# Optimization experiments

Hardware: AMD Instinct MI355X
Metric: run time of the kernel (lower is better)

Reference implementation:

```python
import jax, jax.numpy as jnp
import numpy as np

CTX = (16, 16)          # rel_pos_ctx_size
N_HEADS = 12
HEAD_DIM = 64           # emb_dim // n_heads


def _make_rel_pos_ids(ctx):
    # Faithful replication of the torch buffer construction.
    rge = [2 * s - 1 for s in ctx]
    coords = np.stack(np.meshgrid(*[np.arange(s) for s in ctx], indexing='ij'))  # [2, *ctx]
    coords = coords.reshape(len(ctx), -1)                                        # [2, n]
    rel = coords[:, :, None] - coords[:, None, :]                                # [2, n, n]
    rel = rel.reshape(len(ctx), -1)                                              # [2, n*n]
    rel = rel + (np.array(ctx)[:, None] - 1)
    ids = np.ravel_multi_index(tuple(rel), tuple(rge))                           # [n*n]
    return jnp.asarray(ids, dtype=jnp.int32)


def setup_inputs() -> dict:
    key = jax.random.key(0)
    ks = jax.random.split(key, 6)
    b, n, e = 128, 256, 768
    std_in = 1.0 / np.sqrt(e)
    return {
        'x': jax.random.normal(ks[0], (b, n, e), jnp.float32),
        'W_qkv': jax.random.normal(ks[1], (e, 3 * e), jnp.float32) * std_in,
        'b_qkv': jax.random.normal(ks[2], (3 * e,), jnp.float32) * 0.02,
        'W_out': jax.random.normal(ks[3], (e, e), jnp.float32) * std_in,
        'b_out': jax.random.normal(ks[4], (e,), jnp.float32) * 0.02,
        'rel_bias_table': jax.random.normal(ks[5], ((2 * CTX[0] - 1) * (2 * CTX[1] - 1), N_HEADS), jnp.float32) * 0.02,
        'rel_pos_ids': _make_rel_pos_ids(CTX),
    }


def reference(x, W_qkv, b_qkv, W_out, b_out, rel_bias_table, rel_pos_ids):
    b, n, e = x.shape
    h, d = N_HEADS, HEAD_DIM
    scale = d ** -0.5
    # fused qkv projection: 'b n (k h d) -> k b h n d'
    qkv = (x @ W_qkv + b_qkv).reshape(b, n, 3, h, d)
    q, k, v = (jnp.transpose(qkv, (2, 0, 3, 1, 4))[i] for i in range(3))  # each [b h n d]
    # gathered relative-position bias: [n*n, h] -> [h, n, n]
    bias = rel_bias_table[rel_pos_ids].reshape(n, n, h).transpose(2, 0, 1)
    scores = jnp.einsum('bhnd,bhmd->bhnm', q, k) * scale + bias
    attn = jax.nn.softmax(scores, axis=-1)
    out = jnp.einsum('bhnm,bhmd->bhnd', attn, v)
    out = out.transpose(0, 2, 1, 3).reshape(b, n, e)  # 'b h n d -> b n (h d)'
    return out @ W_out + b_out
```

## Files before the change

### kernel.cpp

```cpp
#include <hip/hip_runtime.h>
#include <cstdint>
#include <cstddef>

typedef __bf16 bf16x8 __attribute__((ext_vector_type(8)));
typedef __bf16 bf16x4 __attribute__((ext_vector_type(4)));
typedef float f32x4 __attribute__((ext_vector_type(4)));
static_assert(sizeof(bf16x8) == 16, "bf16x8 must be 16B");
static_assert(sizeof(bf16x4) == 8, "bf16x4 must be 8B");
static_assert(sizeof(f32x4) == 16, "f32x4 must be 16B");

#define MFMA16(a, b, c) __builtin_amdgcn_mfma_f32_16x16x32_bf16((a), (b), (c), 0, 0, 0)
#define SBAR() __builtin_amdgcn_s_barrier()
#define LGKM0() asm volatile("s_waitcnt lgkmcnt(0)" ::: "memory")
#define VMCNT(n_) asm volatile("s_waitcnt vmcnt(" #n_ ")" ::: "memory")

__device__ __forceinline__ void gload_lds16(const void* g, void* l) {
  __builtin_amdgcn_global_load_lds(
      (const __attribute__((address_space(1))) void*)g,
      (__attribute__((address_space(3))) void*)l, 16, 0, 0);
}

__global__ __launch_bounds__(256) void prep_kernel(
    const float* __restrict__ x, __bf16* __restrict__ xbf,
    const float* __restrict__ Wqkv, __bf16* __restrict__ wqkvt,
    const float* __restrict__ Wout, __bf16* __restrict__ woutt,
    const float* __restrict__ table, const int* __restrict__ ids,
    float* __restrict__ biasT) {
  __shared__ float tile[32][33];
  const int bid = blockIdx.x;
  const int tid = threadIdx.x;

  if (bid < 24576) {
    size_t i = ((size_t)bid * 256 + tid) * 4;
    const float4 v = *(const float4*)(x + i);
    bf16x4 pk;
    pk[0] = (__bf16)v.x;
    pk[1] = (__bf16)v.y;
    pk[2] = (__bf16)v.z;
    pk[3] = (__bf16)v.w;
    *(bf16x4*)(xbf + i) = pk;
  } else if (bid < 26880) {
    const bool big = bid < 26304;
    const int b2 = big ? (bid - 24576) : (bid - 26304);
    const int nt = big ? 72 : 24;
    const int N = big ? 2304 : 768;
    const float* in = big ? Wqkv : Wout;
    __bf16* out = big ? wqkvt : woutt;
    const int n0 = (b2 % nt) * 32, k0 = (b2 / nt) * 32;
    const int tx = tid & 31, ty = tid >> 5;
#pragma unroll
    for (int i = 0; i < 4; ++i)
      tile[ty * 4 + i][tx] = in[(size_t)(k0 + ty * 4 + i) * N + n0 + tx];
    __syncthreads();
#pragma unroll
    for (int i = 0; i < 4; ++i)
      out[(size_t)(n0 + ty * 4 + i) * 768 + k0 + tx] = (__bf16)tile[tx][ty * 4 + i];
  } else {
    const int idx = (bid - 26880) * 256 + tid;
    const int h = idx >> 16, ji = idx & 65535;
    const int j = ji >> 8, i = ji & 255;
    biasT[idx] = table[ids[i * 256 + j] * 12 + h];
  }
}

template <int NT>
__global__ __launch_bounds__(512, 2) void gemm8_qkv_kernel(const __bf16* __restrict__ A,
                                                           const __bf16* __restrict__ Bt,
                                                           const float* __restrict__ bias,
                                                           __bf16* __restrict__ qb,
                                                           __bf16* __restrict__ kb,
                                                           __bf16* __restrict__ vt,
                                                           const int M, const int K) {
  __shared__ __align__(16) __bf16 smem[65536];
  const int tid = threadIdx.x;
  const int lane = tid & 63, w = tid >> 6;
  const int m16 = lane & 15, q4 = lane >> 4;
  const int wm = w & 1, wn = w >> 1;

  const int nwg = NT * (M >> 8);
  const int chunk = nwg >> 3;
  const int id = blockIdx.x;
  const int wg = (id & 7) * chunk + (id >> 3);
  const int mi = wg / NT, ni = wg - mi * NT;
  const int m0 = mi << 8, n0 = ni << 8;

  const int srow = w * 8 + (lane >> 3);
  const int sg = ((lane & 7) ^ (srow & 7)) * 8;
  const __bf16* ag = A + (size_t)(m0 + srow) * K + sg;
  const __bf16* bg = Bt + (size_t)(n0 + srow) * K + sg;
  const int dstw = w * 512;

  const int g0 = (q4 ^ (m16 & 7)) * 8;
  const int g1 = ((4 + q4) ^ (m16 & 7)) * 8;
  const int abase = (wm * 128 + m16) * 64;
  const int bbase = 16384 + (wn * 64 + m16) * 64;

  const int nt = K >> 6;

#define STAGE(T_, mat_, h_)                                                         \
  do {                                                                              \
    const __bf16* s_ = ((mat_) ? bg : ag) + (size_t)(T_)*64 + (size_t)(h_)*128 * K; \
    __bf16* d_ = &smem[((T_)&1) * 32768 + (mat_)*16384 + (h_)*8192 + dstw];         \
    gload_lds16(s_, d_);                                                            \
    gload_lds16(s_ + (size_t)64 * K, d_ + 4096);                                    \
  } while (0)

  STAGE(0, 0, 0);
  STAGE(0, 0, 1);
  STAGE(0, 1, 0);
  STAGE(0, 1, 1);
  STAGE(1, 0, 0);
  VMCNT(2);
  SBAR();

  f32x4 acc[8][4] = {};
  for (int T = 0; T < nt; ++T) {
    const int base = (T & 1) * 32768;
    bf16x8 a[4][2], b0[2][2], b1[2][2];

#pragma unroll
    for (int fm = 0; fm < 4; ++fm) {
      a[fm][0] = *(const bf16x8*)&smem[base + abase + fm * 1024 + g0];
      a[fm][1] = *(const bf16x8*)&smem[base + abase + fm * 1024 + g1];
    }
#pragma unroll
    for (int fn = 0; fn < 2; ++fn) {
      b0[fn][0] = *(const bf16x8*)&smem[base + bbase + fn * 1024 + g0];
      b0[fn][1] = *(const bf16x8*)&smem[base + bbase + fn * 1024 + g1];
    }
    if (T + 1 < nt) {
      STAGE(T + 1, 0, 1);
      STAGE(T + 1, 1, 0);
      STAGE(T + 1, 1, 1);
    }
    SBAR();
    LGKM0();
    __builtin_amdgcn_s_setprio(1);
#pragma unroll
    for (int kh = 0; kh < 2; ++kh)
#pragma unroll
      for (int fm = 0; fm < 4; ++fm)
#pragma unroll
        for (int fn = 0; fn < 2; ++fn)
          acc[fm][fn] = MFMA16(b0[fn][kh], a[fm][kh], acc[fm][fn]);
    __builtin_amdgcn_s_setprio(0);
    SBAR();

#pragma unroll
    for (int fn = 0; fn < 2; ++fn) {
      b1[fn][0] = *(const bf16x8*)&smem[base + bbase + 2048 + fn * 1024 + g0];
      b1[fn][1] = *(const bf16x8*)&smem[base + bbase + 2048 + fn * 1024 + g1];
    }
    SBAR();
    LGKM0();
    __builtin_amdgcn_s_setprio(1);
#pragma unroll
    for (int kh = 0; kh < 2; ++kh)
#pragma unroll
      for (int fm = 0; fm < 4; ++fm)
#pragma unroll
        for (int fn = 0; fn < 2; ++fn)
          acc[fm][2 + fn] = MFMA16(b1[fn][kh], a[fm][kh], acc[fm][2 + fn]);
    __builtin_amdgcn_s_setprio(0);
    SBAR();

#pragma unroll
    for (int fm = 0; fm < 4; ++fm) {
      a[fm][0] = *(const bf16x8*)&smem[base + abase + 4096 + fm * 1024 + g0];
      a[fm][1] = *(const bf16x8*)&smem[base + abase + 4096 + fm * 1024 + g1];
    }
    SBAR();
    LGKM0();
    __builtin_amdgcn_s_setprio(1);
#pragma unroll
    for (int kh = 0; kh < 2; ++kh)
#pragma unroll
      for (int fm = 0; fm < 4; ++fm)
#pragma unroll
        for (int fn = 0; fn < 2; ++fn)
          acc[4 + fm][2 + fn] = MFMA16(b1[fn][kh], a[fm][kh], acc[4 + fm][2 + fn]);
    __builtin_amdgcn_s_setprio(0);
    SBAR();

    if (T + 2 < nt) {
      STAGE(T + 2, 0, 0);
      VMCNT(2);
    } else if (T + 1 < nt) {
      VMCNT(0);
    }
    SBAR();
    __builtin_amdgcn_s_setprio(1);
#pragma unroll
    for (int kh = 0; kh < 2; ++kh)
#pragma unroll
      for (int fm = 0; fm < 4; ++fm)
#pragma unroll
        for (int fn = 0; fn < 2; ++fn)
          acc[4 + fm][fn] = MFMA16(b0[fn][kh], a[fm][kh], acc[4 + fm][fn]);
    __builtin_amdgcn_s_setprio(0);
    SBAR();
  }
#undef STAGE

  __syncthreads();
  const int bi = m0 >> 8;
  char* eb = (char*)smem;

  if (n0 < 1536) {
    const int which = (n0 >= 768);
    const float qscale = which ? 1.0f : 0.125f;
#pragma unroll
    for (int fn = 0; fn < 4; ++fn) {
      const int nloc = wn * 64 + fn * 16 + q4 * 4;
      const f32x4 bn = *(const f32x4*)&bias[n0 + nloc];
      const int cb = nloc * 2;
      const int slot = cb >> 4;
      const int half8 = cb & 15;
#pragma unroll
      for (int fm = 0; fm < 8; ++fm) {
        const int tok = wm * 128 + fm * 16 + m16;
        bf16x4 pk;
#pragma unroll
        for (int r = 0; r < 4; ++r) pk[r] = (__bf16)((acc[fm][fn][r] + bn[r]) * qscale);
        *(bf16x4*)(eb + tok * 512 + ((slot ^ (tok & 7)) << 4) + half8) = pk;
      }
    }
    __syncthreads();
    const int nrel0 = n0 - which * 768;
    __bf16* dst = (which ? kb : qb) + (size_t)bi * 12 * 16384;
#pragma unroll
    for (int pass = 0; pass < 16; ++pass) {
      const int tokr = pass * 16 + (tid >> 5);
      const int slot = tid & 31;
      const bf16x8 vv = *(const bf16x8*)(eb + tokr * 512 + ((slot ^ (tokr & 7)) << 4));
      const int nr = nrel0 + slot * 8;
      *(bf16x8*)(dst + (size_t)(nr >> 6) * 16384 + (size_t)tokr * 64 + (nr & 63)) = vv;
    }
  } else {
#pragma unroll
    for (int fn = 0; fn < 4; ++fn)
#pragma unroll
      for (int r = 0; r < 4; ++r) {
        const int nloc = wn * 64 + fn * 16 + q4 * 4 + r;
        const float bn = bias[n0 + nloc];
#pragma unroll
        for (int fm = 0; fm < 8; ++fm) {
          const int tok = wm * 128 + fm * 16 + m16;
          const int tcb = tok * 2;
          *(__bf16*)(eb + nloc * 512 + (((tcb >> 4) ^ (nloc & 7)) << 4) + (tcb & 15)) =
              (__bf16)(acc[fm][fn][r] + bn);
        }
      }
    __syncthreads();
    const int nrel0v = n0 - 1536;
#pragma unroll
    for (int pass = 0; pass < 16; ++pass) {
      const int nr = pass * 16 + (tid >> 5);
      const int slot = tid & 31;
      const bf16x8 vv = *(const bf16x8*)(eb + nr * 512 + ((slot ^ (nr & 7)) << 4));
      const int ng = nrel0v + nr;
      *(bf16x8*)(vt + (((size_t)bi * 12 + (ng >> 6)) * 64 + (ng & 63)) * 256 + slot * 8) = vv;
    }
  }
}

template <int NT>
__global__ __launch_bounds__(512, 2) void gemm8_out_kernel(const __bf16* __restrict__ A,
                                                           const __bf16* __restrict__ Bt,
                                                           const float* __restrict__ bias,
                                                           float* __restrict__ out,
                                                           const int M, const int N,
                                                           const int K) {
  __shared__ __align__(16) __bf16 smem[65536];
  const int tid = threadIdx.x;
  const int lane = tid & 63, w = tid >> 6;
  const int m16 = lane & 15, q4 = lane >> 4;
  const int wm = w & 1, wn = w >> 1;

  const int nwg = NT * (M >> 8);
  const int chunk = nwg >> 3;
  const int id = blockIdx.x;
  const int wg = (id & 7) * chunk + (id >> 3);
  const int mi = wg / NT, ni = wg - mi * NT;
  const int m0 = mi << 8, n0 = ni << 8;

  const int srow = w * 8 + (lane >> 3);
  const int sg = ((lane & 7) ^ (srow & 7)) * 8;
  const __bf16* ag = A + (size_t)(m0 + srow) * K + sg;
  const __bf16* bg = Bt + (size_t)(n0 + srow) * K + sg;
  const int dstw = w * 512;

  const int g0 = (q4 ^ (m16 & 7)) * 8;
  const int g1 = ((4 + q4) ^ (m16 & 7)) * 8;
  const int abase = (wm * 128 + m16) * 64;
  const int bbase = 16384 + (wn * 64 + m16) * 64;

  const int nt = K >> 6;

#define STAGE(T_, mat_, h_)                                                         \
  do {                                                                              \
    const __bf16* s_ = ((mat_) ? bg : ag) + (size_t)(T_)*64 + (size_t)(h_)*128 * K; \
    __bf16* d_ = &smem[((T_)&1) * 32768 + (mat_)*16384 + (h_)*8192 + dstw];         \
    gload_lds16(s_, d_);                                                            \
    gload_lds16(s_ + (size_t)64 * K, d_ + 4096);                                    \
  } while (0)

  STAGE(0, 0, 0);
  STAGE(0, 0, 1);
  STAGE(0, 1, 0);
  STAGE(0, 1, 1);
  STAGE(1, 0, 0);
  VMCNT(2);
  SBAR();

  f32x4 acc[8][4] = {};
  for (int T = 0; T < nt; ++T) {
    const int base = (T & 1) * 32768;
    bf16x8 a[4][2], b0[2][2], b1[2][2];

#pragma unroll
    for (int fm = 0; fm < 4; ++fm) {
      a[fm][0] = *(const bf16x8*)&smem[base + abase + fm * 1024 + g0];
      a[fm][1] = *(const bf16x8*)&smem[base + abase + fm * 1024 + g1];
    }
#pragma unroll
    for (int fn = 0; fn < 2; ++fn) {
      b0[fn][0] = *(const bf16x8*)&smem[base + bbase + fn * 1024 + g0];
      b0[fn][1] = *(const bf16x8*)&smem[base + bbase + fn * 1024 + g1];
    }
    if (T + 1 < nt) {
      STAGE(T + 1, 0, 1);
      STAGE(T + 1, 1, 0);
      STAGE(T + 1, 1, 1);
    }
    SBAR();
    LGKM0();
    __builtin_amdgcn_s_setprio(1);
#pragma unroll
    for (int kh = 0; kh < 2; ++kh)
#pragma unroll
      for (int fm = 0; fm < 4; ++fm)
#pragma unroll
        for (int fn = 0; fn < 2; ++fn)
          acc[fm][fn] = MFMA16(b0[fn][kh], a[fm][kh], acc[fm][fn]);
    __builtin_amdgcn_s_setprio(0);
    SBAR();

#pragma unroll
    for (int fn = 0; fn < 2; ++fn) {
      b1[fn][0] = *(const bf16x8*)&smem[base + bbase + 2048 + fn * 1024 + g0];
      b1[fn][1] = *(const bf16x8*)&smem[base + bbase + 2048 + fn * 1024 + g1];
    }
    SBAR();
    LGKM0();
    __builtin_amdgcn_s_setprio(1);
#pragma unroll
    for (int kh = 0; kh < 2; ++kh)
#pragma unroll
      for (int fm = 0; fm < 4; ++fm)
#pragma unroll
        for (int fn = 0; fn < 2; ++fn)
          acc[fm][2 + fn] = MFMA16(b1[fn][kh], a[fm][kh], acc[fm][2 + fn]);
    __builtin_amdgcn_s_setprio(0);
    SBAR();

#pragma unroll
    for (int fm = 0; fm < 4; ++fm) {
      a[fm][0] = *(const bf16x8*)&smem[base + abase + 4096 + fm * 1024 + g0];
      a[fm][1] = *(const bf16x8*)&smem[base + abase + 4096 + fm * 1024 + g1];
    }
    SBAR();
    LGKM0();
    __builtin_amdgcn_s_setprio(1);
#pragma unroll
    for (int kh = 0; kh < 2; ++kh)
#pragma unroll
      for (int fm = 0; fm < 4; ++fm)
#pragma unroll
        for (int fn = 0; fn < 2; ++fn)
          acc[4 + fm][2 + fn] = MFMA16(b1[fn][kh], a[fm][kh], acc[4 + fm][2 + fn]);
    __builtin_amdgcn_s_setprio(0);
    SBAR();

    if (T + 2 < nt) {
      STAGE(T + 2, 0, 0);
      VMCNT(2);
    } else if (T + 1 < nt) {
      VMCNT(0);
    }
    SBAR();
    __builtin_amdgcn_s_setprio(1);
#pragma unroll
    for (int kh = 0; kh < 2; ++kh)
#pragma unroll
      for (int fm = 0; fm < 4; ++fm)
#pragma unroll
        for (int fn = 0; fn < 2; ++fn)
          acc[4 + fm][fn] = MFMA16(b0[fn][kh], a[fm][kh], acc[4 + fm][fn]);
    __builtin_amdgcn_s_setprio(0);
    SBAR();
  }
#undef STAGE

  __syncthreads();
  char* ef = (char*)smem;
#pragma unroll
  for (int half = 0; half < 2; ++half) {
    if ((wn >> 1) == half) {
#pragma unroll
      for (int fn = 0; fn < 4; ++fn) {
        const int nl = (wn & 1) * 64 + fn * 16 + q4 * 4;
        const f32x4 bn = *(const f32x4*)&bias[n0 + half * 128 + nl];
        const int slot = nl >> 2;
#pragma unroll
        for (int fm = 0; fm < 8; ++fm) {
          const int tok = wm * 128 + fm * 16 + m16;
          f32x4 v;
#pragma unroll
          for (int r = 0; r < 4; ++r) v[r] = acc[fm][fn][r] + bn[r];
          *(f32x4*)(ef + tok * 512 + ((slot ^ (tok & 7)) << 4)) = v;
        }
      }
    }
    __syncthreads();
#pragma unroll
    for (int pass = 0; pass < 16; ++pass) {
      const int tokr = pass * 16 + (tid >> 5);
      const int slot = tid & 31;
      const f32x4 vv = *(const f32x4*)(ef + tokr * 512 + ((slot ^ (tokr & 7)) << 4));
      *(f32x4*)(out + (size_t)(m0 + tokr) * N + n0 + half * 128 + slot * 4) = vv;
    }
    __syncthreads();
  }
}

__global__ __launch_bounds__(512, 4) void attn_kernel(const __bf16* __restrict__ qb,
                                                      const __bf16* __restrict__ kb,
                                                      const __bf16* __restrict__ vtb,
                                                      const float* __restrict__ biasT,
                                                      __bf16* __restrict__ o_ws) {
  __shared__ __bf16 klds[256 * 64];
  __shared__ __bf16 vlds[64 * 256];
  const int tid = threadIdx.x;
  const int lane = tid & 63, w = tid >> 6;
  const int m16 = lane & 15, q4 = lane >> 4;
  const int b = blockIdx.x, h = blockIdx.y;
  const size_t bh = (size_t)b * 12 + h;
  const __bf16* Q = qb + bh * (256 * 64);
  const __bf16* Kp = kb + bh * (256 * 64);
  const __bf16* Vt = vtb + bh * (64 * 256);
  const float* BhT = biasT + (size_t)h * 65536;
  const int qbase = blockIdx.z * 128;
  const int qrow0 = qbase + w * 16;

#pragma unroll
  for (int i = 0; i < 4; ++i) {
    const int row = w * 32 + i * 8 + (lane >> 3);
    const int col = ((lane & 7) ^ (row & 7)) * 8;
    gload_lds16(Kp + (size_t)row * 64 + col, &klds[(w * 32 + i * 8) * 64]);
  }
#pragma unroll
  for (int i = 0; i < 4; ++i) {
    const int row = w * 8 + i * 2 + (lane >> 5);
    const int g = lane & 31;
    const int gp = (g & 24) | ((g & 7) ^ (row & 7));
    gload_lds16(Vt + (size_t)row * 256 + gp * 8, &vlds[(w * 8 + i * 2) * 256]);
  }

  bf16x8 qf[2];
#pragma unroll
  for (int t = 0; t < 2; ++t)
    qf[t] = *(const bf16x8*)(Q + (size_t)(qrow0 + m16) * 64 + t * 32 + q4 * 8);

  __syncthreads();

  f32x4 s[16];
#pragma unroll
  for (int c = 0; c < 16; ++c) {
    const int krow = c * 16 + m16;
    const bf16x8 kf0 = *(const bf16x8*)&klds[krow * 64 + ((q4 ^ (m16 & 7)) * 8)];
    const bf16x8 kf1 = *(const bf16x8*)&klds[krow * 64 + (((4 + q4) ^ (m16 & 7)) * 8)];
    f32x4 z = {0.f, 0.f, 0.f, 0.f};
    z = MFMA16(qf[0], kf0, z);
    s[c] = MFMA16(qf[1], kf1, z);
  }

#pragma unroll
  for (int c = 0; c < 16; ++c) {
    const f32x4 bv = *(const f32x4*)&BhT[(size_t)(c * 16 + m16) * 256 + qrow0 + q4 * 4];
    s[c] += bv;
  }

  float linv[4];
#pragma unroll
  for (int r = 0; r < 4; ++r) {
    float mx = s[0][r];
#pragma unroll
    for (int c = 1; c < 16; ++c) mx = fmaxf(mx, s[c][r]);
    mx = fmaxf(mx, __shfl_xor(mx, 1));
    mx = fmaxf(mx, __shfl_xor(mx, 2));
    mx = fmaxf(mx, __shfl_xor(mx, 4));
    mx = fmaxf(mx, __shfl_xor(mx, 8));
    float sum = 0.f;
#pragma unroll
    for (int c = 0; c < 16; ++c) {
      const float p = __builtin_amdgcn_exp2f((s[c][r] - mx) * 1.4426950408889634f);
      s[c][r] = p;
      sum += p;
    }
    sum += __shfl_xor(sum, 1);
    sum += __shfl_xor(sum, 2);
    sum += __shfl_xor(sum, 4);
    sum += __shfl_xor(sum, 8);
    linv[r] = 1.f / sum;
  }

  __syncthreads();

  f32x4 o[4] = {};
  __bf16* P = &klds[w * 1152];
#pragma unroll
  for (int ch = 0; ch < 4; ++ch) {
#pragma unroll
    for (int cc = 0; cc < 4; ++cc)
#pragma unroll
      for (int r = 0; r < 4; ++r)
        P[(q4 * 4 + r) * 72 + cc * 16 + m16] = (__bf16)s[ch * 4 + cc][r];
#pragma unroll
    for (int kt = 0; kt < 2; ++kt) {
      const bf16x8 pf = *(const bf16x8*)(P + m16 * 72 + kt * 32 + q4 * 8);
#pragma unroll
      for (int dt = 0; dt < 4; ++dt) {
        const int vrow = dt * 16 + m16;
        const bf16x8 vf = *(const bf16x8*)&vlds[vrow * 256 + ch * 64 +
                                                (((kt * 4 + q4) ^ (m16 & 7)) * 8)];
        o[dt] = MFMA16(pf, vf, o[dt]);
      }
    }
  }

#pragma unroll
  for (int dt = 0; dt < 4; ++dt)
#pragma unroll
    for (int r = 0; r < 4; ++r) {
      const float v = o[dt][r] * linv[r];
      const size_t row = (size_t)b * 256 + qrow0 + q4 * 4 + r;
      o_ws[row * 768 + h * 64 + dt * 16 + m16] = (__bf16)v;
    }
}

extern "C" void kernel_launch(void* const* d_in, const int* in_sizes, int n_in,
                              void* d_out, int out_size, void* d_ws, size_t ws_size,
                              hipStream_t stream) {
  const float* x = (const float*)d_in[0];
  const float* Wqkv = (const float*)d_in[1];
  const float* bqkv = (const float*)d_in[2];
  const float* Wout = (const float*)d_in[3];
  const float* bout = (const float*)d_in[4];
  const float* table = (const float*)d_in[5];
  const int* ids = (const int*)d_in[6];
  float* out = (float*)d_out;

  char* ws = (char*)d_ws;
  __bf16* xbf = (__bf16*)ws;
  __bf16* wqkvt = (__bf16*)(ws + 50331648);
  __bf16* woutt = (__bf16*)(ws + 53870592);
  __bf16* qbuf = (__bf16*)(ws + 55050240);
  __bf16* kbuf = (__bf16*)(ws + 105381888);
  __bf16* vtbuf = (__bf16*)(ws + 155713536);
  float* biasT = (float*)(ws + 206045184);

  prep_kernel<<<29952, 256, 0, stream>>>(x, xbf, Wqkv, wqkvt, Wout, woutt,
                                         table, ids, biasT);
  gemm8_qkv_kernel<9><<<1152, 512, 0, stream>>>(xbf, wqkvt, bqkv, qbuf, kbuf, vtbuf,
                                                32768, 768);
  attn_kernel<<<dim3(128, 12, 2), 512, 0, stream>>>(qbuf, kbuf, vtbuf, biasT, xbf );
  gemm8_out_kernel<3><<<384, 512, 0, stream>>>(xbf, woutt, bout, out, 32768, 768, 768);
}
```

Before: 460.3 us.

## Widen x conversion, fold log2e into Q scale and bias, use nontemporal stores

The x fp32-to-bf16 conversion now handles 8 elements per thread, so the prep grid shrinks from 29952 to 17664 blocks. The log2(e) factor is folded into the Q scale and the bias table, which removes one multiply per element from the softmax exp. The Q, K and V^T stores, the attention output and the final output now use nontemporal stores to reduce cache pollution. Rounding Q to bf16 after the extra scale changes numerics slightly, and nontemporal stores of data that the next kernel reads back may lose L2/MALL reuse.

```diff
diff --git a/kernel.cpp b/kernel.cpp
--- a/kernel.cpp
+++ b/kernel.cpp
@@ -13,6 +13,8 @@
 #define SBAR() __builtin_amdgcn_s_barrier()
 #define LGKM0() asm volatile("s_waitcnt lgkmcnt(0)" ::: "memory")
 #define VMCNT(n_) asm volatile("s_waitcnt vmcnt(" #n_ ")" ::: "memory")
+
+#define LOG2E 1.4426950408889634f
 
 __device__ __forceinline__ void gload_lds16(const void* g, void* l) {
   __builtin_amdgcn_global_load_lds(
@@ -30,18 +32,19 @@
   const int bid = blockIdx.x;
   const int tid = threadIdx.x;
 
-  if (bid < 24576) {
-    size_t i = ((size_t)bid * 256 + tid) * 4;
-    const float4 v = *(const float4*)(x + i);
-    bf16x4 pk;
-    pk[0] = (__bf16)v.x;
-    pk[1] = (__bf16)v.y;
-    pk[2] = (__bf16)v.z;
-    pk[3] = (__bf16)v.w;
-    *(bf16x4*)(xbf + i) = pk;
-  } else if (bid < 26880) {
-    const bool big = bid < 26304;
-    const int b2 = big ? (bid - 24576) : (bid - 26304);
+  if (bid < 12288) {
+    size_t i = ((size_t)bid * 256 + tid) * 8;
+    const float4 v0 = *(const float4*)(x + i);
+    const float4 v1 = *(const float4*)(x + i + 4);
+    bf16x8 pk;
+    pk[0] = (__bf16)v0.x; pk[1] = (__bf16)v0.y;
+    pk[2] = (__bf16)v0.z; pk[3] = (__bf16)v0.w;
+    pk[4] = (__bf16)v1.x; pk[5] = (__bf16)v1.y;
+    pk[6] = (__bf16)v1.z; pk[7] = (__bf16)v1.w;
+    *(bf16x8*)(xbf + i) = pk;
+  } else if (bid < 14592) {
+    const bool big = bid < 14016;
+    const int b2 = big ? (bid - 12288) : (bid - 14016);
     const int nt = big ? 72 : 24;
     const int N = big ? 2304 : 768;
     const float* in = big ? Wqkv : Wout;
@@ -56,10 +59,10 @@
     for (int i = 0; i < 4; ++i)
       out[(size_t)(n0 + ty * 4 + i) * 768 + k0 + tx] = (__bf16)tile[tx][ty * 4 + i];
   } else {
-    const int idx = (bid - 26880) * 256 + tid;
+    const int idx = (bid - 14592) * 256 + tid;
     const int h = idx >> 16, ji = idx & 65535;
     const int j = ji >> 8, i = ji & 255;
-    biasT[idx] = table[ids[i * 256 + j] * 12 + h];
+    biasT[idx] = table[ids[i * 256 + j] * 12 + h] * LOG2E;
   }
 }
 
@@ -208,7 +211,7 @@
 
   if (n0 < 1536) {
     const int which = (n0 >= 768);
-    const float qscale = which ? 1.0f : 0.125f;
+    const float qscale = which ? 1.0f : 0.125f * LOG2E;
 #pragma unroll
     for (int fn = 0; fn < 4; ++fn) {
       const int nloc = wn * 64 + fn * 16 + q4 * 4;
@@ -234,7 +237,8 @@
       const int slot = tid & 31;
       const bf16x8 vv = *(const bf16x8*)(eb + tokr * 512 + ((slot ^ (tokr & 7)) << 4));
       const int nr = nrel0 + slot * 8;
-      *(bf16x8*)(dst + (size_t)(nr >> 6) * 16384 + (size_t)tokr * 64 + (nr & 63)) = vv;
+      __builtin_nontemporal_store(
+          vv, (bf16x8*)(dst + (size_t)(nr >> 6) * 16384 + (size_t)tokr * 64 + (nr & 63)));
     }
   } else {
 #pragma unroll
@@ -259,7 +263,9 @@
       const int slot = tid & 31;
       const bf16x8 vv = *(const bf16x8*)(eb + nr * 512 + ((slot ^ (nr & 7)) << 4));
       const int ng = nrel0v + nr;
-      *(bf16x8*)(vt + (((size_t)bi * 12 + (ng >> 6)) * 64 + (ng & 63)) * 256 + slot * 8) = vv;
+      __builtin_nontemporal_store(
+          vv, (bf16x8*)(vt + (((size_t)bi * 12 + (ng >> 6)) * 64 + (ng & 63)) * 256 +
+                        slot * 8));
     }
   }
 }
@@ -428,7 +434,8 @@
       const int tokr = pass * 16 + (tid >> 5);
       const int slot = tid & 31;
       const f32x4 vv = *(const f32x4*)(ef + tokr * 512 + ((slot ^ (tokr & 7)) << 4));
-      *(f32x4*)(out + (size_t)(m0 + tokr) * N + n0 + half * 128 + slot * 4) = vv;
+      __builtin_nontemporal_store(
+          vv, (f32x4*)(out + (size_t)(m0 + tokr) * N + n0 + half * 128 + slot * 4));
     }
     __syncthreads();
   }
@@ -504,7 +511,7 @@
     float sum = 0.f;
 #pragma unroll
     for (int c = 0; c < 16; ++c) {
-      const float p = __builtin_amdgcn_exp2f((s[c][r] - mx) * 1.4426950408889634f);
+      const float p = __builtin_amdgcn_exp2f(s[c][r] - mx);
       s[c][r] = p;
       sum += p;
     }
@@ -545,7 +552,8 @@
     for (int r = 0; r < 4; ++r) {
       const float v = o[dt][r] * linv[r];
       const size_t row = (size_t)b * 256 + qrow0 + q4 * 4 + r;
-      o_ws[row * 768 + h * 64 + dt * 16 + m16] = (__bf16)v;
+      __builtin_nontemporal_store((__bf16)v,
+                                  o_ws + row * 768 + h * 64 + dt * 16 + m16);
     }
 }
 
@@ -570,7 +578,7 @@
   __bf16* vtbuf = (__bf16*)(ws + 155713536);
   float* biasT = (float*)(ws + 206045184);
 
-  prep_kernel<<<29952, 256, 0, stream>>>(x, xbf, Wqkv, wqkvt, Wout, woutt,
+  prep_kernel<<<17664, 256, 0, stream>>>(x, xbf, Wqkv, wqkvt, Wout, woutt,
                                          table, ids, biasT);
   gemm8_qkv_kernel<9><<<1152, 512, 0, stream>>>(xbf, wqkvt, bqkv, qbuf, kbuf, vtbuf,
                                                 32768, 768);
```

After: 487.6 us. +5.9%, slower.
